# Performance work log

Hardware: AMD Instinct MI355X
Metric: run time of the kernel (lower is better)

## Reference

```python
import jax, jax.numpy as jnp
import numpy as np

D_MODEL = 1024
NUM_HEADS = 16
D_K = D_MODEL // NUM_HEADS


def setup_inputs() -> dict:
    key = jax.random.key(0)
    kq, kwq, kwk, kwv, kwo = jax.random.split(key, 5)
    B, S = 4, 2048
    Q = jax.random.normal(kq, (B, S, D_MODEL), dtype=jnp.float32)
    # causal mask, broadcastable to (B, H, Sq, Sk); mask==0 -> -1e9
    mask = jnp.tril(jnp.ones((S, S), dtype=jnp.int32))[None, None]
    scale = 1.0 / np.sqrt(D_MODEL)
    W_q = jax.random.normal(kwq, (D_MODEL, D_MODEL), dtype=jnp.float32) * scale
    W_k = jax.random.normal(kwk, (D_MODEL, D_MODEL), dtype=jnp.float32) * scale
    W_v = jax.random.normal(kwv, (D_MODEL, D_MODEL), dtype=jnp.float32) * scale
    W_o = jax.random.normal(kwo, (D_MODEL, D_MODEL), dtype=jnp.float32) * scale
    return {"Q": Q, "W_q": W_q, "W_k": W_k, "W_v": W_v, "W_o": W_o, "mask": mask}


def _split_heads(x):
    B, S, _ = x.shape
    return x.reshape(B, S, NUM_HEADS, D_K).transpose(0, 2, 1, 3)  # (B,H,S,Dk)


def reference(Q, W_q, W_k, W_v, W_o, mask):
    # self-attention path: K = V = Q (inputs), dropout=0 (identity)
    q = _split_heads(Q @ W_q.T)
    k = _split_heads(Q @ W_k.T)
    v = _split_heads(Q @ W_v.T)
    scores = jnp.einsum('bhqd,bhkd->bhqk', q, k) / jnp.sqrt(jnp.float32(D_K))
    scores = jnp.where(mask == 0, jnp.float32(-1e9), scores)
    attn = jax.nn.softmax(scores, axis=-1)
    out = jnp.einsum('bhqk,bhkd->bhqd', attn, v)  # (B,H,S,Dk)
    B, H, S, Dk = out.shape
    out = out.transpose(0, 2, 1, 3).reshape(B, S, H * Dk)
    return out @ W_o.T
```

## Files before the change

### kernel.cpp

```cpp
#include <hip/hip_runtime.h>
#include <hip/hip_bf16.h>
#include <stdint.h>

typedef __attribute__((ext_vector_type(8))) short s8v;
typedef __attribute__((ext_vector_type(4))) float f4v;
typedef __attribute__((ext_vector_type(4))) unsigned short us4v;
typedef __attribute__((ext_vector_type(2))) unsigned int u32x2;

#define MFMA16(a,b,c) __builtin_amdgcn_mfma_f32_16x16x32_bf16((a),(b),(c),0,0,0)

__device__ __forceinline__ unsigned short bfu(float x){
  __hip_bfloat16 h = __float2bfloat16(x);
  return __builtin_bit_cast(unsigned short, h);
}

__device__ __forceinline__ void gload_lds16(const void* g, void* l){
  __builtin_amdgcn_global_load_lds((const __attribute__((address_space(1))) unsigned int*)g,
                                   (__attribute__((address_space(3))) unsigned int*)l,
                                   16, 0, 0);
}

__global__ __launch_bounds__(256) void k_convert(
    const float* __restrict__ Q,  const float* __restrict__ W0,
    const float* __restrict__ W1, const float* __restrict__ W2,
    const float* __restrict__ W3, unsigned short* __restrict__ dst){
  int t = blockIdx.x*256 + threadIdx.x;
  int e = t*4;
  const float* src; int off;
  if (e < 8388608)       { src = Q;  off = e; }
  else if (e < 9437184)  { src = W0; off = e - 8388608; }
  else if (e < 10485760) { src = W1; off = e - 9437184; }
  else if (e < 11534336) { src = W2; off = e - 10485760; }
  else                   { src = W3; off = e - 11534336; }
  float4 v = *(const float4*)(src + off);
  us4v o = { bfu(v.x), bfu(v.y), bfu(v.z), bfu(v.w) };
  *(us4v*)(dst + e) = o;
}

__device__ __forceinline__ void gemm_core(const unsigned short* __restrict__ A,
                                          const unsigned short* __restrict__ B,
                                          int m0, int n0, unsigned short* lds,
                                          f4v acc[4][4]){
  const int tid = threadIdx.x, wave = tid>>6, lane = tid&63, lq = lane&15, g = lane>>4;
  const int wr = wave>>1, wc = wave&1;
  char* ldsA = (char*)lds;
  char* ldsB = (char*)lds + 8192;
  for (int kt = 0; kt < 1024; kt += 32){
    __syncthreads();
    #pragma unroll
    for (int i = 0; i < 2; ++i){
      int L = (i*256 + tid)*16;
      int row = L>>6, ssw = (L>>4)&3;
      int gcol = kt + ((ssw ^ (row&3))<<3);
      gload_lds16(A + (m0 + row)*1024 + gcol, ldsA + i*4096 + wave*1024);
      gload_lds16(B + (n0 + row)*1024 + gcol, ldsB + i*4096 + wave*1024);
    }
    __syncthreads();
    s8v af[4], bf[4];
    #pragma unroll
    for (int mi = 0; mi < 4; ++mi){
      int row = wr*64 + mi*16 + lq;
      af[mi] = *(const s8v*)(ldsA + row*64 + ((g ^ (row&3))<<4));
    }
    #pragma unroll
    for (int ni = 0; ni < 4; ++ni){
      int row = wc*64 + ni*16 + lq;
      bf[ni] = *(const s8v*)(ldsB + row*64 + ((g ^ (row&3))<<4));
    }
    #pragma unroll
    for (int mi = 0; mi < 4; ++mi)
      #pragma unroll
      for (int ni = 0; ni < 4; ++ni)
        acc[mi][ni] = MFMA16(af[mi], bf[ni], acc[mi][ni]);
  }
}

__global__ __launch_bounds__(256) void k_qkv(
    const unsigned short* __restrict__ xb,
    const unsigned short* __restrict__ wq, const unsigned short* __restrict__ wk,
    const unsigned short* __restrict__ wv,
    unsigned short* __restrict__ qb, unsigned short* __restrict__ kb,
    unsigned short* __restrict__ vtb){
  __shared__ unsigned short lds[8192];
  const int m0 = blockIdx.x*128;
  const int by = blockIdx.y, wsel = by>>3, n0 = (by&7)*128;
  const unsigned short* B = (wsel==0)? wq : ((wsel==1)? wk : wv);
  f4v acc[4][4] = {};
  gemm_core(xb, B, m0, n0, lds, acc);
  const int tid = threadIdx.x, wave = tid>>6, lane = tid&63, lq = lane&15, g = lane>>4;
  const int wr = wave>>1, wc = wave&1;
  #pragma unroll
  for (int mi = 0; mi < 4; ++mi){
    int mbase = m0 + wr*64 + mi*16 + g*4;
    int b = mbase>>11, s = mbase&2047;
    #pragma unroll
    for (int ni = 0; ni < 4; ++ni){
      int n = n0 + wc*64 + ni*16 + lq;
      int h = n>>6, d = n&63;
      f4v a = acc[mi][ni];
      if (wsel == 2){
        us4v p = { bfu(a[0]), bfu(a[1]), bfu(a[2]), bfu(a[3]) };
        *(us4v*)(vtb + ((b*16 + h)*64 + d)*2048 + s) = p;
      } else {
        unsigned short* dst = wsel ? kb : qb;
        int base = ((b*16 + h)*2048 + s)*64 + d;
        dst[base      ] = bfu(a[0]);
        dst[base +  64] = bfu(a[1]);
        dst[base + 128] = bfu(a[2]);
        dst[base + 192] = bfu(a[3]);
      }
    }
  }
}

#define CSCL 0.18033688011112042f
__global__ __launch_bounds__(256, 2) void k_attn(
    const unsigned short* __restrict__ qbuf, const unsigned short* __restrict__ kbuf,
    const unsigned short* __restrict__ vtbuf, unsigned short* __restrict__ ao){
  __shared__ unsigned short lds[32768];
  char* ldsK = (char*)lds;
  char* ldsV = (char*)lds + 16384;
  const int tid = threadIdx.x, wave = tid>>6, lane = tid&63, lq = lane&15, g = lane>>4;
  char* ldsP = (char*)lds + 32768 + wave*8192;
  const int bh = blockIdx.x;
  const int qt = 15 - blockIdx.y;
  const int qbase = qt*128;
  const unsigned short* qh = qbuf  + bh*131072;
  const unsigned short* kh = kbuf  + bh*131072;
  const unsigned short* vh = vtbuf + bh*131072;

  s8v qf_[2][2];
  #pragma unroll
  for (int qf = 0; qf < 2; ++qf)
    #pragma unroll
    for (int ks = 0; ks < 2; ++ks){
      int row = qbase + wave*32 + qf*16 + lq;
      qf_[qf][ks] = *(const s8v*)(qh + row*64 + ks*32 + g*8);
    }

  f4v ot[4][2] = {};
  float mrow[2] = {-INFINITY, -INFINITY};
  float lrow[2] = {0.f, 0.f};

  for (int kt = 0; kt <= qt; ++kt){
    int kbase = kt*128;
    __syncthreads();
    #pragma unroll
    for (int i = 0; i < 4; ++i){
      int L = (i*256 + tid)*16;
      { int row = L>>7, ssw = (L>>4)&7;
        gload_lds16(kh + (kbase + row)*64 + ((ssw ^ (row&7))<<3),
                    ldsK + i*4096 + wave*1024); }
      { int d = L>>8, ssw = (L>>4)&15;
        gload_lds16(vh + d*2048 + kbase + ((ssw ^ (d&7))<<3),
                    ldsV + i*4096 + wave*1024); }
    }
    __syncthreads();

    f4v sf[8][2];
    #pragma unroll
    for (int kf = 0; kf < 8; ++kf){
      s8v ka[2];
      #pragma unroll
      for (int ks = 0; ks < 2; ++ks){
        int row = kf*16 + lq;
        ka[ks] = *(const s8v*)(ldsK + row*128 + (((4*ks + g) ^ (row&7))<<4));
      }
      #pragma unroll
      for (int qf = 0; qf < 2; ++qf){
        f4v s = {};
        s = MFMA16(ka[0], qf_[qf][0], s);
        s = MFMA16(ka[1], qf_[qf][1], s);
        sf[kf][qf] = s;
      }
    }

    #pragma unroll
    for (int qf = 0; qf < 2; ++qf){
      int qg = qbase + wave*32 + qf*16 + lq;
      if (kt == qt){
        #pragma unroll
        for (int kf = 0; kf < 8; ++kf)
          #pragma unroll
          for (int i = 0; i < 4; ++i){
            int kgl = kbase + kf*16 + g*4 + i;
            if (kgl > qg) sf[kf][qf][i] = -1e30f;
          }
      }
      float tm = -INFINITY;
      #pragma unroll
      for (int kf = 0; kf < 8; ++kf){
        f4v s = sf[kf][qf];
        tm = fmaxf(tm, fmaxf(fmaxf(s[0], s[1]), fmaxf(s[2], s[3])));
      }
      tm = fmaxf(tm, __shfl_xor(tm, 16));
      tm = fmaxf(tm, __shfl_xor(tm, 32));
      float mnew = fmaxf(mrow[qf], tm);
      float alpha = exp2f((mrow[qf] - mnew)*CSCL);
      mrow[qf] = mnew;
      float nm = mnew*CSCL;
      float ps = 0.f;
      int q_l = qf*16 + lq;
      #pragma unroll
      for (int kf = 0; kf < 8; ++kf){
        f4v s = sf[kf][qf];
        float p0 = exp2f(fmaf(s[0], CSCL, -nm));
        float p1 = exp2f(fmaf(s[1], CSCL, -nm));
        float p2 = exp2f(fmaf(s[2], CSCL, -nm));
        float p3 = exp2f(fmaf(s[3], CSCL, -nm));
        ps += (p0+p1) + (p2+p3);
        unsigned int lo = (unsigned int)bfu(p0) | ((unsigned int)bfu(p1)<<16);
        unsigned int hi = (unsigned int)bfu(p2) | ((unsigned int)bfu(p3)<<16);
        int k0 = kf*16 + g*4;
        int byte = q_l*256 + (((k0>>3) ^ (q_l&7))<<4) + ((k0&7)<<1);
        u32x2 pk = { lo, hi };
        *(u32x2*)(ldsP + byte) = pk;
      }
      ps += __shfl_xor(ps, 16);
      ps += __shfl_xor(ps, 32);
      lrow[qf] = lrow[qf]*alpha + ps;
      #pragma unroll
      for (int df = 0; df < 4; ++df)
        #pragma unroll
        for (int i = 0; i < 4; ++i)
          ot[df][qf][i] *= alpha;
    }

    #pragma unroll
    for (int ks = 0; ks < 4; ++ks){
      s8v va[4], pb[2];
      #pragma unroll
      for (int df = 0; df < 4; ++df){
        int row = df*16 + lq;
        va[df] = *(const s8v*)(ldsV + row*256 + (((4*ks + g) ^ (row&7))<<4));
      }
      #pragma unroll
      for (int qf = 0; qf < 2; ++qf){
        int q_l = qf*16 + lq;
        pb[qf] = *(const s8v*)(ldsP + q_l*256 + (((4*ks + g) ^ (q_l&7))<<4));
      }
      #pragma unroll
      for (int df = 0; df < 4; ++df)
        #pragma unroll
        for (int qf = 0; qf < 2; ++qf)
          ot[df][qf] = MFMA16(va[df], pb[qf], ot[df][qf]);
    }
  }

  const int b = bh>>4, h = bh&15;
  #pragma unroll
  for (int qf = 0; qf < 2; ++qf){
    float rin = 1.f / lrow[qf];
    int qg = qbase + wave*32 + qf*16 + lq;
    int rowoff = (b*2048 + qg)*1024 + h*64;
    #pragma unroll
    for (int df = 0; df < 4; ++df){
      f4v o = ot[df][qf];
      us4v p = { bfu(o[0]*rin), bfu(o[1]*rin), bfu(o[2]*rin), bfu(o[3]*rin) };
      *(us4v*)(ao + rowoff + df*16 + g*4) = p;
    }
  }
}

__global__ __launch_bounds__(256) void k_out(
    const unsigned short* __restrict__ aob, const unsigned short* __restrict__ wo,
    float* __restrict__ out){
  __shared__ unsigned short lds[8192];
  const int m0 = blockIdx.x*128, n0 = blockIdx.y*128;
  f4v acc[4][4] = {};
  gemm_core(aob, wo, m0, n0, lds, acc);
  const int tid = threadIdx.x, wave = tid>>6, lane = tid&63, lq = lane&15, g = lane>>4;
  const int wr = wave>>1, wc = wave&1;
  #pragma unroll
  for (int mi = 0; mi < 4; ++mi){
    int mbase = m0 + wr*64 + mi*16 + g*4;
    #pragma unroll
    for (int ni = 0; ni < 4; ++ni){
      int n = n0 + wc*64 + ni*16 + lq;
      f4v a = acc[mi][ni];
      #pragma unroll
      for (int i = 0; i < 4; ++i)
        out[(mbase + i)*1024 + n] = a[i];
    }
  }
}

extern "C" void kernel_launch(void* const* d_in, const int* in_sizes, int n_in,
                              void* d_out, int out_size, void* d_ws, size_t ws_size,
                              hipStream_t stream){
  const float* Q  = (const float*)d_in[0];
  const float* Wq = (const float*)d_in[1];
  const float* Wk = (const float*)d_in[2];
  const float* Wv = (const float*)d_in[3];
  const float* Wo = (const float*)d_in[4];

  unsigned short* ws   = (unsigned short*)d_ws;
  unsigned short* xb   = ws;
  unsigned short* wqb  = ws + 8388608;
  unsigned short* wkb  = ws + 9437184;
  unsigned short* wvb  = ws + 10485760;
  unsigned short* wob  = ws + 11534336;
  unsigned short* qbuf = ws + 12582912;
  unsigned short* kbuf = ws + 20971520;
  unsigned short* vtb  = ws + 29360128;
  unsigned short* aob  = ws;

  k_convert<<<12288, 256, 0, stream>>>(Q, Wq, Wk, Wv, Wo, ws);
  k_qkv<<<dim3(64, 24), 256, 0, stream>>>(xb, wqb, wkb, wvb, qbuf, kbuf, vtb);
  k_attn<<<dim3(64, 16), 256, 0, stream>>>(qbuf, kbuf, vtb, aob);
  k_out<<<dim3(64, 8), 256, 0, stream>>>(aob, wob, (float*)d_out);
}
```

Before: 276.0 us.

## Shrink attention LDS for 3 blocks/CU, add lazy rescale and fast exp2

Attention's per-wave P buffer is halved by processing one 16-row query fragment at a time through PV, cutting LDS so launch bounds can request three blocks per CU. Online softmax now keeps the max in scaled units and only rescales O and l when the new max exceeds the old one by more than 8 (warp-uniform check), which skips most rescale work. exp2f is replaced by the hardware exp2 builtin, and the GEMM LDS swizzle uses (row>>1)&3 to reduce bank conflicts. The tradeoffs are more register pressure under the higher occupancy target, V fragments being reloaded per query fragment, and less precise exp.

```diff
diff --git a/kernel.cpp b/kernel.cpp
--- a/kernel.cpp
+++ b/kernel.cpp
@@ -8,6 +8,12 @@
 typedef __attribute__((ext_vector_type(2))) unsigned int u32x2;
 
 #define MFMA16(a,b,c) __builtin_amdgcn_mfma_f32_16x16x32_bf16((a),(b),(c),0,0,0)
+
+#if __has_builtin(__builtin_amdgcn_exp2f)
+#define EXP2(x) __builtin_amdgcn_exp2f(x)
+#else
+#define EXP2(x) exp2f(x)
+#endif
 
 __device__ __forceinline__ unsigned short bfu(float x){
   __hip_bfloat16 h = __float2bfloat16(x);
@@ -51,7 +57,7 @@
     for (int i = 0; i < 2; ++i){
       int L = (i*256 + tid)*16;
       int row = L>>6, ssw = (L>>4)&3;
-      int gcol = kt + ((ssw ^ (row&3))<<3);
+      int gcol = kt + ((ssw ^ ((row>>1)&3))<<3);
       gload_lds16(A + (m0 + row)*1024 + gcol, ldsA + i*4096 + wave*1024);
       gload_lds16(B + (n0 + row)*1024 + gcol, ldsB + i*4096 + wave*1024);
     }
@@ -60,12 +66,12 @@
     #pragma unroll
     for (int mi = 0; mi < 4; ++mi){
       int row = wr*64 + mi*16 + lq;
-      af[mi] = *(const s8v*)(ldsA + row*64 + ((g ^ (row&3))<<4));
+      af[mi] = *(const s8v*)(ldsA + row*64 + ((g ^ ((row>>1)&3))<<4));
     }
     #pragma unroll
     for (int ni = 0; ni < 4; ++ni){
       int row = wc*64 + ni*16 + lq;
-      bf[ni] = *(const s8v*)(ldsB + row*64 + ((g ^ (row&3))<<4));
+      bf[ni] = *(const s8v*)(ldsB + row*64 + ((g ^ ((row>>1)&3))<<4));
     }
     #pragma unroll
     for (int mi = 0; mi < 4; ++mi)
@@ -114,14 +120,14 @@
 }
 
 #define CSCL 0.18033688011112042f
-__global__ __launch_bounds__(256, 2) void k_attn(
+__global__ __launch_bounds__(256, 3) void k_attn(
     const unsigned short* __restrict__ qbuf, const unsigned short* __restrict__ kbuf,
     const unsigned short* __restrict__ vtbuf, unsigned short* __restrict__ ao){
-  __shared__ unsigned short lds[32768];
+  __shared__ unsigned short lds[24576];
   char* ldsK = (char*)lds;
   char* ldsV = (char*)lds + 16384;
   const int tid = threadIdx.x, wave = tid>>6, lane = tid&63, lq = lane&15, g = lane>>4;
-  char* ldsP = (char*)lds + 32768 + wave*8192;
+  char* ldsP = (char*)lds + 32768 + wave*4096;
   const int bh = blockIdx.x;
   const int qt = 15 - blockIdx.y;
   const int qbase = qt*128;
@@ -195,55 +201,52 @@
       }
       tm = fmaxf(tm, __shfl_xor(tm, 16));
       tm = fmaxf(tm, __shfl_xor(tm, 32));
-      float mnew = fmaxf(mrow[qf], tm);
-      float alpha = exp2f((mrow[qf] - mnew)*CSCL);
-      mrow[qf] = mnew;
-      float nm = mnew*CSCL;
+      float tms = tm*CSCL;
+      if (!__all(tms <= mrow[qf] + 8.0f)){
+        float mnew = fmaxf(mrow[qf], tms);
+        float alpha = EXP2(mrow[qf] - mnew);
+        mrow[qf] = mnew;
+        lrow[qf] *= alpha;
+        #pragma unroll
+        for (int df = 0; df < 4; ++df)
+          #pragma unroll
+          for (int i = 0; i < 4; ++i)
+            ot[df][qf][i] *= alpha;
+      }
+      float nm = mrow[qf];
       float ps = 0.f;
-      int q_l = qf*16 + lq;
       #pragma unroll
       for (int kf = 0; kf < 8; ++kf){
         f4v s = sf[kf][qf];
-        float p0 = exp2f(fmaf(s[0], CSCL, -nm));
-        float p1 = exp2f(fmaf(s[1], CSCL, -nm));
-        float p2 = exp2f(fmaf(s[2], CSCL, -nm));
-        float p3 = exp2f(fmaf(s[3], CSCL, -nm));
+        float p0 = EXP2(fmaf(s[0], CSCL, -nm));
+        float p1 = EXP2(fmaf(s[1], CSCL, -nm));
+        float p2 = EXP2(fmaf(s[2], CSCL, -nm));
+        float p3 = EXP2(fmaf(s[3], CSCL, -nm));
         ps += (p0+p1) + (p2+p3);
         unsigned int lo = (unsigned int)bfu(p0) | ((unsigned int)bfu(p1)<<16);
         unsigned int hi = (unsigned int)bfu(p2) | ((unsigned int)bfu(p3)<<16);
         int k0 = kf*16 + g*4;
-        int byte = q_l*256 + (((k0>>3) ^ (q_l&7))<<4) + ((k0&7)<<1);
+        int byte = lq*256 + (((k0>>3) ^ (lq&7))<<4) + ((k0&7)<<1);
         u32x2 pk = { lo, hi };
         *(u32x2*)(ldsP + byte) = pk;
       }
       ps += __shfl_xor(ps, 16);
       ps += __shfl_xor(ps, 32);
-      lrow[qf] = lrow[qf]*alpha + ps;
-      #pragma unroll
-      for (int df = 0; df < 4; ++df)
+      lrow[qf] += ps;
+
+      #pragma unroll
+      for (int ks = 0; ks < 4; ++ks){
+        s8v va[4], pb;
         #pragma unroll
-        for (int i = 0; i < 4; ++i)
-          ot[df][qf][i] *= alpha;
-    }
-
-    #pragma unroll
-    for (int ks = 0; ks < 4; ++ks){
-      s8v va[4], pb[2];
-      #pragma unroll
-      for (int df = 0; df < 4; ++df){
-        int row = df*16 + lq;
-        va[df] = *(const s8v*)(ldsV + row*256 + (((4*ks + g) ^ (row&7))<<4));
-      }
-      #pragma unroll
-      for (int qf = 0; qf < 2; ++qf){
-        int q_l = qf*16 + lq;
-        pb[qf] = *(const s8v*)(ldsP + q_l*256 + (((4*ks + g) ^ (q_l&7))<<4));
-      }
-      #pragma unroll
-      for (int df = 0; df < 4; ++df)
+        for (int df = 0; df < 4; ++df){
+          int row = df*16 + lq;
+          va[df] = *(const s8v*)(ldsV + row*256 + (((4*ks + g) ^ (row&7))<<4));
+        }
+        pb = *(const s8v*)(ldsP + lq*256 + (((4*ks + g) ^ (lq&7))<<4));
         #pragma unroll
-        for (int qf = 0; qf < 2; ++qf)
-          ot[df][qf] = MFMA16(va[df], pb[qf], ot[df][qf]);
+        for (int df = 0; df < 4; ++df)
+          ot[df][qf] = MFMA16(va[df], pb, ot[df][qf]);
+      }
     }
   }
 
```

Measured after the change: 293.4 us. 6.3% more time.
